# Kernel optimization log

Measured on AMD Instinct MI355X. Metric: run time of the kernel, lower is better.

Reference implementation:

```python
import jax, jax.numpy as jnp
import numpy as np
from jax import lax

KERNEL_SIZE = 2
DILATION = 1


def setup_inputs() -> dict:
    key = jax.random.key(0)
    k1, k2, k3, k4, k5 = jax.random.split(key, 5)
    bsz, h_size, seq_len = 8, 1024, 1024
    z1ss = jax.random.normal(k1, (bsz, 2 * h_size, seq_len), dtype=jnp.float32)
    uss = jax.random.normal(k2, (bsz, 4 * h_size, seq_len), dtype=jnp.float32)
    z0 = jax.random.normal(k3, (bsz, 2 * h_size, 1), dtype=jnp.float32)
    # conv params initialized ~ N(0, 0.01) as in init_weights
    weight = 0.01 * jax.random.normal(k4, (4 * h_size, h_size, KERNEL_SIZE), dtype=jnp.float32)
    bias = 0.01 * jax.random.normal(k5, (4 * h_size,), dtype=jnp.float32)
    return {"z1ss": z1ss, "uss": uss, "z0": z0, "weight": weight, "bias": bias}


def reference(z1ss, uss, z0, weight, bias):
    h_size = z1ss.shape[1] // 2
    z1h, z1c = z1ss[:, :h_size], z1ss[:, h_size:]          # (B, H, T) each
    z0h, z0c0 = z0[:, :h_size], z0[:, h_size:]             # (B, H, 1)
    # previous cell state: [z0c, z1c[..., :-1]]
    z0c = jnp.concatenate([z0c0, z1c], axis=2)[:, :, :-1]  # (B, H, T)
    # causal pad, injecting hid into the padded region
    pad = (KERNEL_SIZE - 1) * DILATION
    b = z1h.shape[0]
    hid = jnp.broadcast_to(z0h, (b, h_size, pad))
    xp = jnp.concatenate([hid, z1h], axis=2)               # (B, H, T+pad)
    conv = lax.conv_general_dilated(
        xp, weight, window_strides=(1,), padding='VALID',
        rhs_dilation=(DILATION,), dimension_numbers=('NCH', 'OIH', 'NCH'))
    out = uss + conv + bias[None, :, None]                 # (B, 4H, T)
    it, ot, gt, ft = jnp.split(out, 4, axis=1)
    it, ot, gt, ft = jax.nn.sigmoid(it), jax.nn.sigmoid(ot), jnp.tanh(gt), jax.nn.sigmoid(ft)
    ct = ft * z0c + it * gt
    ht = ot * jnp.tanh(ct)
    return jnp.concatenate([ht, ct], axis=1)               # (B, 2H, T)
```

## Files before the change

### kernel.cpp

```cpp
#include <hip/hip_runtime.h>
#include <hip/hip_bf16.h>
#include <cstdint>

#define HSZ   1024
#define SEQ   1024
#define NTOT  8192
#define K2    2048

typedef __attribute__((ext_vector_type(8))) short bf16x8;
typedef __attribute__((ext_vector_type(4))) float f32x4;

__device__ __forceinline__ unsigned f2bf(float x) {
  unsigned u = __builtin_bit_cast(unsigned, x);
  return (u + 0x7fffu + ((u >> 16) & 1u)) >> 16;
}
__device__ __forceinline__ float fsig(float x)  { return 1.f / (1.f + __expf(-x)); }
__device__ __forceinline__ float ftanh(float x) { return 1.f - 2.f / (__expf(2.f * x) + 1.f); }

__device__ __forceinline__ void gload_lds16(const void* g, void* l) {
  __builtin_amdgcn_global_load_lds(
      (const __attribute__((address_space(1))) unsigned*)g,
      (__attribute__((address_space(3))) unsigned*)l, 16, 0, 0);
}

__global__ void conv_weight_kernel(const float* __restrict__ w, unsigned* __restrict__ wb) {
  const int idx = (blockIdx.x * 256 + threadIdx.x) * 8;
  f32x4 a = *(const f32x4*)(w + idx);
  f32x4 c = *(const f32x4*)(w + idx + 4);
  uint4 o;
  o.x = f2bf(a.x) | (f2bf(a.y) << 16);
  o.y = f2bf(a.z) | (f2bf(a.w) << 16);
  o.z = f2bf(c.x) | (f2bf(c.y) << 16);
  o.w = f2bf(c.z) | (f2bf(c.w) << 16);
  *(uint4*)(wb + (idx >> 1)) = o;
}

__global__ void build_bdup_kernel(const float* __restrict__ z1ss, const float* __restrict__ z0,
                                  unsigned* __restrict__ bd) {
  __shared__ float tile[32 * 65];
  const int tid = threadIdx.x;
  const int n0 = blockIdx.x * 64;
  const int i0 = blockIdx.y * 32;
  const int b  = n0 >> 10;
  const int t0 = n0 & 1023;
  const int l16 = tid & 15, r16 = tid >> 4;
#pragma unroll
  for (int pr = 0; pr < 2; ++pr) {
    const int ii = r16 + pr * 16;
    const float* zrow = z1ss + (size_t)(b * 2048 + i0 + ii) * 1024;
    f32x4 v = *(const f32x4*)(zrow + t0 + l16 * 4);
    float* tr = tile + ii * 65 + 1 + l16 * 4;
    tr[0] = v.x; tr[1] = v.y; tr[2] = v.z; tr[3] = v.w;
    if (l16 == 0)
      tile[ii * 65] = t0 ? zrow[t0 - 1] : z0[b * 2048 + i0 + ii];
  }
  __syncthreads();
  const int i2 = tid & 31, ts = tid >> 5;
#pragma unroll
  for (int p = 0; p < 8; ++p) {
    const int tt = ts + p * 8;
    float prev = tile[i2 * 65 + tt];
    float cur  = tile[i2 * 65 + tt + 1];
    bd[(size_t)(n0 + tt) * 1024 + i0 + i2] = f2bf(prev) | (f2bf(cur) << 16);
  }
}

__launch_bounds__(256, 3)
__global__ void lstm_gemm_kernel(const unsigned short* __restrict__ Wb,
                                 const unsigned short* __restrict__ Bd,
                                 const float* __restrict__ uss,
                                 const float* __restrict__ z1ss,
                                 const float* __restrict__ z0,
                                 const float* __restrict__ bias,
                                 float* __restrict__ out) {
  __shared__ unsigned short Asm_[128 * 64];
  __shared__ unsigned short Bsm_[128 * 64];
  const int tid  = threadIdx.x;
  const int wave = tid >> 6, lane = tid & 63;
  const int l15  = lane & 15, quad = lane >> 4;
  const int c0 = blockIdx.y * 32;
  const int n0 = blockIdx.x * 128;

  const unsigned short* agp[4];
  const unsigned short* bgp[4];
#pragma unroll
  for (int j = 0; j < 4; ++j) {
    const int idx = (wave * 4 + j) * 64 + lane;
    const int row = idx >> 3;
    const int chunk = (idx & 7) ^ (row & 7);
    const int wrow = (row >> 5) * 1024 + c0 + (row & 31);
    agp[j] = Wb + (size_t)wrow * K2 + chunk * 8;
    bgp[j] = Bd + (size_t)(n0 + row) * K2 + chunk * 8;
  }
  unsigned short* ldsA[4];
  unsigned short* ldsB[4];
#pragma unroll
  for (int j = 0; j < 4; ++j) {
    ldsA[j] = Asm_ + (wave * 4 + j) * 512;
    ldsB[j] = Bsm_ + (wave * 4 + j) * 512;
  }

  const int sw7 = l15 & 7;

  f32x4 acc[4][2][2];
#pragma unroll
  for (int g = 0; g < 4; ++g)
#pragma unroll
    for (int h = 0; h < 2; ++h)
#pragma unroll
      for (int nt = 0; nt < 2; ++nt)
        acc[g][h][nt] = (f32x4){0.f, 0.f, 0.f, 0.f};

  for (int k0 = 0; k0 < K2; k0 += 64) {
#pragma unroll
    for (int j = 0; j < 4; ++j) gload_lds16(agp[j] + k0, ldsA[j]);
#pragma unroll
    for (int j = 0; j < 4; ++j) gload_lds16(bgp[j] + k0, ldsB[j]);
    __syncthreads();

#pragma unroll
    for (int kh = 0; kh < 2; ++kh) {
      const int slot = ((kh * 4 + quad) ^ sw7) << 3;
      bf16x8 bf[2];
#pragma unroll
      for (int nt = 0; nt < 2; ++nt) {
        const int br = wave * 32 + nt * 16 + l15;
        bf[nt] = *(const bf16x8*)(Bsm_ + br * 64 + slot);
      }
#pragma unroll
      for (int g = 0; g < 4; ++g)
#pragma unroll
        for (int h = 0; h < 2; ++h) {
          const int ar = (g * 2 + h) * 16 + l15;
          bf16x8 af = *(const bf16x8*)(Asm_ + ar * 64 + slot);
#pragma unroll
          for (int nt = 0; nt < 2; ++nt)
            acc[g][h][nt] = __builtin_amdgcn_mfma_f32_16x16x32_bf16(af, bf[nt], acc[g][h][nt], 0, 0, 0);
        }
    }
    __syncthreads();
  }

#pragma unroll
  for (int h = 0; h < 2; ++h) {
#pragma unroll
    for (int r = 0; r < 4; ++r) {
      const int c = c0 + h * 16 + quad * 4 + r;
      const float bv0 = bias[c], bv1 = bias[1024 + c], bv2 = bias[2048 + c], bv3 = bias[3072 + c];
#pragma unroll
      for (int nt = 0; nt < 2; ++nt) {
        const int n = n0 + wave * 32 + nt * 16 + l15;
        const int b = n >> 10, t = n & 1023;
        const int ub = b * 4194304 + c * 1024 + t;
        float p0 = acc[0][h][nt][r] + uss[ub]           + bv0;
        float p1 = acc[1][h][nt][r] + uss[ub + 1048576] + bv1;
        float p2 = acc[2][h][nt][r] + uss[ub + 2097152] + bv2;
        float p3 = acc[3][h][nt][r] + uss[ub + 3145728] + bv3;
        float it = fsig(p0), ot = fsig(p1), g_ = ftanh(p2), ft = fsig(p3);
        float zc = t ? z1ss[(b * 2048 + 1024 + c) * 1024 + t - 1]
                     : z0[b * 2048 + 1024 + c];
        float ct = ft * zc + it * g_;
        float ht = ot * ftanh(ct);
        const int ob = (b * 2048 + c) * 1024 + t;
        out[ob] = ht;
        out[ob + 1048576] = ct;
      }
    }
  }
}

__global__ void naive_kernel(const float* __restrict__ z1ss, const float* __restrict__ uss,
                             const float* __restrict__ z0, const float* __restrict__ w,
                             const float* __restrict__ bias, float* __restrict__ out) {
  int idx = blockIdx.x * 256 + threadIdx.x;
  int b = idx >> 20, c = (idx >> 10) & 1023, t = idx & 1023;
  float s0 = 0.f, s1 = 0.f, s2 = 0.f, s3 = 0.f;
  const float* xb = z1ss + b * 2097152;
  for (int i = 0; i < 1024; ++i) {
    float cur  = xb[i * 1024 + t];
    float prev = t ? xb[i * 1024 + t - 1] : z0[b * 2048 + i];
    const float* wr = w + c * 2048 + i * 2;
    s0 += wr[0]       * prev + wr[1]       * cur;
    s1 += wr[2097152] * prev + wr[2097153] * cur;
    s2 += wr[4194304] * prev + wr[4194305] * cur;
    s3 += wr[6291456] * prev + wr[6291457] * cur;
  }
  int ub = b * 4194304 + c * 1024 + t;
  float p0 = s0 + uss[ub]           + bias[c];
  float p1 = s1 + uss[ub + 1048576] + bias[1024 + c];
  float p2 = s2 + uss[ub + 2097152] + bias[2048 + c];
  float p3 = s3 + uss[ub + 3145728] + bias[3072 + c];
  float it = fsig(p0), ot = fsig(p1), g_ = ftanh(p2), ft = fsig(p3);
  float zc = t ? z1ss[(b * 2048 + 1024 + c) * 1024 + t - 1] : z0[b * 2048 + 1024 + c];
  float ct = ft * zc + it * g_;
  float ht = ot * ftanh(ct);
  int ob = (b * 2048 + c) * 1024 + t;
  out[ob] = ht;
  out[ob + 1048576] = ct;
}

extern "C" void kernel_launch(void* const* d_in, const int* in_sizes, int n_in,
                              void* d_out, int out_size, void* d_ws, size_t ws_size,
                              hipStream_t stream) {
  const float* z1ss = (const float*)d_in[0];
  const float* uss  = (const float*)d_in[1];
  const float* z0   = (const float*)d_in[2];
  const float* w    = (const float*)d_in[3];
  const float* bias = (const float*)d_in[4];
  float* out = (float*)d_out;

  const size_t needWb = (size_t)4096 * 2048 * 2;
  const size_t needBd = (size_t)NTOT * K2 * 2;
  if (ws_size >= needWb + needBd) {
    unsigned short* Wb = (unsigned short*)d_ws;
    unsigned short* Bd = Wb + (size_t)4096 * 2048;
    conv_weight_kernel<<<4096, 256, 0, stream>>>(w, (unsigned*)Wb);
    build_bdup_kernel<<<dim3(128, 32), 256, 0, stream>>>(z1ss, z0, (unsigned*)Bd);
    lstm_gemm_kernel<<<dim3(64, 32), 256, 0, stream>>>(Wb, Bd, uss, z1ss, z0, bias, out);
  } else {
    naive_kernel<<<32768, 256, 0, stream>>>(z1ss, uss, z0, w, bias, out);
  }
}
```

Baseline: 400.9 us.

## Interleave gate weight rows and use 2x2 wave tiling for GEMM

The bf16 weight is repacked so the four gate rows of each channel sit next to each other (row = 4*c + gate). Each MFMA accumulator then holds all four gates for one channel in its four registers. The waves are rearranged from a 1x4 split along N into a 2x2 grid, each owning 64x64. This changes per-wave LDS fragment reuse from 8 A plus 2 B loads to 4 A plus 4 B loads per k-half. The epilogue reads the gates directly from .x/.y/.z/.w, at the cost of changed store access patterns.

```diff
diff --git a/kernel.cpp b/kernel.cpp
--- a/kernel.cpp
+++ b/kernel.cpp
@@ -25,14 +25,18 @@
 
 __global__ void conv_weight_kernel(const float* __restrict__ w, unsigned* __restrict__ wb) {
   const int idx = (blockIdx.x * 256 + threadIdx.x) * 8;
+  const int o  = idx >> 11;
+  const int kk = idx & 2047;
+  const int g = o >> 10, c = o & 1023;
+  const int R = (c << 2) | g;
   f32x4 a = *(const f32x4*)(w + idx);
-  f32x4 c = *(const f32x4*)(w + idx + 4);
-  uint4 o;
-  o.x = f2bf(a.x) | (f2bf(a.y) << 16);
-  o.y = f2bf(a.z) | (f2bf(a.w) << 16);
-  o.z = f2bf(c.x) | (f2bf(c.y) << 16);
-  o.w = f2bf(c.z) | (f2bf(c.w) << 16);
-  *(uint4*)(wb + (idx >> 1)) = o;
+  f32x4 d = *(const f32x4*)(w + idx + 4);
+  uint4 ov;
+  ov.x = f2bf(a.x) | (f2bf(a.y) << 16);
+  ov.y = f2bf(a.z) | (f2bf(a.w) << 16);
+  ov.z = f2bf(d.x) | (f2bf(d.y) << 16);
+  ov.w = f2bf(d.z) | (f2bf(d.w) << 16);
+  *(uint4*)(wb + (((R << 11) | kk) >> 1)) = ov;
 }
 
 __global__ void build_bdup_kernel(const float* __restrict__ z1ss, const float* __restrict__ z0,
@@ -78,6 +82,7 @@
   const int tid  = threadIdx.x;
   const int wave = tid >> 6, lane = tid & 63;
   const int l15  = lane & 15, quad = lane >> 4;
+  const int wm   = wave >> 1, wn = wave & 1;
   const int c0 = blockIdx.y * 32;
   const int n0 = blockIdx.x * 128;
 
@@ -88,8 +93,7 @@
     const int idx = (wave * 4 + j) * 64 + lane;
     const int row = idx >> 3;
     const int chunk = (idx & 7) ^ (row & 7);
-    const int wrow = (row >> 5) * 1024 + c0 + (row & 31);
-    agp[j] = Wb + (size_t)wrow * K2 + chunk * 8;
+    agp[j] = Wb + (size_t)(c0 * 4 + row) * K2 + chunk * 8;
     bgp[j] = Bd + (size_t)(n0 + row) * K2 + chunk * 8;
   }
   unsigned short* ldsA[4];
@@ -102,14 +106,12 @@
 
   const int sw7 = l15 & 7;
 
-  f32x4 acc[4][2][2];
-#pragma unroll
-  for (int g = 0; g < 4; ++g)
-#pragma unroll
-    for (int h = 0; h < 2; ++h)
-#pragma unroll
-      for (int nt = 0; nt < 2; ++nt)
-        acc[g][h][nt] = (f32x4){0.f, 0.f, 0.f, 0.f};
+  f32x4 acc[4][4];
+#pragma unroll
+  for (int m = 0; m < 4; ++m)
+#pragma unroll
+    for (int nt = 0; nt < 4; ++nt)
+      acc[m][nt] = (f32x4){0.f, 0.f, 0.f, 0.f};
 
   for (int k0 = 0; k0 < K2; k0 += 64) {
 #pragma unroll
@@ -121,50 +123,43 @@
 #pragma unroll
     for (int kh = 0; kh < 2; ++kh) {
       const int slot = ((kh * 4 + quad) ^ sw7) << 3;
-      bf16x8 bf[2];
-#pragma unroll
-      for (int nt = 0; nt < 2; ++nt) {
-        const int br = wave * 32 + nt * 16 + l15;
-        bf[nt] = *(const bf16x8*)(Bsm_ + br * 64 + slot);
+      bf16x8 bf[4];
+#pragma unroll
+      for (int nt = 0; nt < 4; ++nt)
+        bf[nt] = *(const bf16x8*)(Bsm_ + (wn * 64 + nt * 16 + l15) * 64 + slot);
+#pragma unroll
+      for (int m = 0; m < 4; ++m) {
+        bf16x8 af = *(const bf16x8*)(Asm_ + (wm * 64 + m * 16 + l15) * 64 + slot);
+#pragma unroll
+        for (int nt = 0; nt < 4; ++nt)
+          acc[m][nt] = __builtin_amdgcn_mfma_f32_16x16x32_bf16(af, bf[nt], acc[m][nt], 0, 0, 0);
       }
-#pragma unroll
-      for (int g = 0; g < 4; ++g)
-#pragma unroll
-        for (int h = 0; h < 2; ++h) {
-          const int ar = (g * 2 + h) * 16 + l15;
-          bf16x8 af = *(const bf16x8*)(Asm_ + ar * 64 + slot);
-#pragma unroll
-          for (int nt = 0; nt < 2; ++nt)
-            acc[g][h][nt] = __builtin_amdgcn_mfma_f32_16x16x32_bf16(af, bf[nt], acc[g][h][nt], 0, 0, 0);
-        }
     }
     __syncthreads();
   }
 
 #pragma unroll
-  for (int h = 0; h < 2; ++h) {
-#pragma unroll
-    for (int r = 0; r < 4; ++r) {
-      const int c = c0 + h * 16 + quad * 4 + r;
-      const float bv0 = bias[c], bv1 = bias[1024 + c], bv2 = bias[2048 + c], bv3 = bias[3072 + c];
-#pragma unroll
-      for (int nt = 0; nt < 2; ++nt) {
-        const int n = n0 + wave * 32 + nt * 16 + l15;
-        const int b = n >> 10, t = n & 1023;
-        const int ub = b * 4194304 + c * 1024 + t;
-        float p0 = acc[0][h][nt][r] + uss[ub]           + bv0;
-        float p1 = acc[1][h][nt][r] + uss[ub + 1048576] + bv1;
-        float p2 = acc[2][h][nt][r] + uss[ub + 2097152] + bv2;
-        float p3 = acc[3][h][nt][r] + uss[ub + 3145728] + bv3;
-        float it = fsig(p0), ot = fsig(p1), g_ = ftanh(p2), ft = fsig(p3);
-        float zc = t ? z1ss[(b * 2048 + 1024 + c) * 1024 + t - 1]
-                     : z0[b * 2048 + 1024 + c];
-        float ct = ft * zc + it * g_;
-        float ht = ot * ftanh(ct);
-        const int ob = (b * 2048 + c) * 1024 + t;
-        out[ob] = ht;
-        out[ob + 1048576] = ct;
-      }
+  for (int m = 0; m < 4; ++m) {
+    const int ch = c0 + wm * 16 + m * 4 + quad;
+    const float bv0 = bias[ch], bv1 = bias[1024 + ch], bv2 = bias[2048 + ch], bv3 = bias[3072 + ch];
+#pragma unroll
+    for (int nt = 0; nt < 4; ++nt) {
+      const int n = n0 + wn * 64 + nt * 16 + l15;
+      const int b = n >> 10, t = n & 1023;
+      const int ub = b * 4194304 + ch * 1024 + t;
+      f32x4 ac = acc[m][nt];
+      float p0 = ac.x + uss[ub]           + bv0;
+      float p1 = ac.y + uss[ub + 1048576] + bv1;
+      float p2 = ac.z + uss[ub + 2097152] + bv2;
+      float p3 = ac.w + uss[ub + 3145728] + bv3;
+      float it = fsig(p0), ot = fsig(p1), g_ = ftanh(p2), ft = fsig(p3);
+      float zc = t ? z1ss[(b * 2048 + 1024 + ch) * 1024 + t - 1]
+                   : z0[b * 2048 + 1024 + ch];
+      float ct = ft * zc + it * g_;
+      float ht = ot * ftanh(ct);
+      const int ob = (b * 2048 + ch) * 1024 + t;
+      out[ob] = ht;
+      out[ob + 1048576] = ct;
     }
   }
 }
```

After: 397.8 us. No clear change (-0.8%).
